# Kernel optimization log

Measured on AMD Instinct MI355X. Metric: run time of the kernel, lower is better.

Reference implementation:

```python
import jax, jax.numpy as jnp
import numpy as np

NUM_TOPICS = 50
NUM_TIMES = 12
VOCAB1 = 5000
VOCAB2 = 2000
T_HIDDEN = 400
RHO = 300
DELTA = 0.005
BATCH = 32


def setup_inputs() -> dict:
    key = jax.random.key(0)
    ks = jax.random.split(key, 16)
    s = 0.02
    V = VOCAB1 + VOCAB2
    d = {}
    d["bows"] = jax.random.uniform(ks[0], (BATCH, NUM_TIMES, V), jnp.float32)
    d["normalized_bows"] = jax.random.uniform(ks[1], (BATCH, NUM_TIMES, V), jnp.float32)
    d["qmap_w"] = jax.random.normal(ks[2], (T_HIDDEN, V), jnp.float32) * s
    d["qmap_b"] = jnp.zeros((T_HIDDEN,), jnp.float32)
    d["lstm_wih0"] = jax.random.normal(ks[3], (4 * T_HIDDEN, T_HIDDEN), jnp.float32) * s
    d["lstm_whh0"] = jax.random.normal(ks[4], (4 * T_HIDDEN, T_HIDDEN), jnp.float32) * s
    d["lstm_bih0"] = jnp.zeros((4 * T_HIDDEN,), jnp.float32)
    d["lstm_bhh0"] = jnp.zeros((4 * T_HIDDEN,), jnp.float32)
    d["lstm_wih1"] = jax.random.normal(ks[5], (4 * T_HIDDEN, T_HIDDEN), jnp.float32) * s
    d["lstm_whh1"] = jax.random.normal(ks[6], (4 * T_HIDDEN, T_HIDDEN), jnp.float32) * s
    d["lstm_bih1"] = jnp.zeros((4 * T_HIDDEN,), jnp.float32)
    d["lstm_bhh1"] = jnp.zeros((4 * T_HIDDEN,), jnp.float32)
    d["mu_theta_w"] = jax.random.normal(ks[7], (NUM_TOPICS, T_HIDDEN + NUM_TOPICS), jnp.float32) * s
    d["mu_theta_b"] = jnp.zeros((NUM_TOPICS,), jnp.float32)
    d["ls_theta_w"] = jax.random.normal(ks[8], (NUM_TOPICS, T_HIDDEN + NUM_TOPICS), jnp.float32) * s
    d["ls_theta_b"] = jnp.zeros((NUM_TOPICS,), jnp.float32)
    d["mu_q_alpha"] = jax.random.normal(ks[9], (NUM_TOPICS, NUM_TIMES, RHO), jnp.float32)
    d["logsigma_q_alpha"] = jax.random.normal(ks[10], (NUM_TOPICS, NUM_TIMES, RHO), jnp.float32)
    d["rho1_w"] = jax.random.normal(ks[11], (VOCAB1, RHO), jnp.float32) * s
    d["rho1_b"] = jnp.zeros((VOCAB1,), jnp.float32)
    d["rho2_w"] = jax.random.normal(ks[12], (VOCAB2, RHO), jnp.float32) * s
    d["rho2_b"] = jnp.zeros((VOCAB2,), jnp.float32)
    return d


def _kl(qm, qls, pm, pls):
    # 0.5 * sum_last[ (exp(qls) + (qm-pm)^2) / (exp(pls)+1e-6) - 1 + pls - qls ], mean over rest
    t = (jnp.exp(qls) + (qm - pm) ** 2) / (jnp.exp(pls) + 1e-6) - 1.0 + pls - qls
    return (0.5 * jnp.sum(t, axis=-1)).mean()


def _lstm(x, layers):
    # x: [B, T, H]; PyTorch gate order i, f, g, o; eval mode -> no inter-layer dropout
    for wih, whh, bih, bhh in layers:
        B = x.shape[0]
        H = whh.shape[1]

        def step(carry, xt, wih=wih, whh=whh, bih=bih, bhh=bhh):
            h, c = carry
            g = xt @ wih.T + bih + h @ whh.T + bhh
            i, f, gg, o = jnp.split(g, 4, axis=-1)
            c = jax.nn.sigmoid(f) * c + jax.nn.sigmoid(i) * jnp.tanh(gg)
            h = jax.nn.sigmoid(o) * jnp.tanh(c)
            return (h, c), h

        init = (jnp.zeros((B, H), x.dtype), jnp.zeros((B, H), x.dtype))
        _, hs = jax.lax.scan(step, init, jnp.swapaxes(x, 0, 1))  # [T, B, H]
        x = jnp.swapaxes(hs, 0, 1)
    return x


def _likelihood(beta, theta, bows_v, key):
    # beta: [T, K, V], theta: [T, B, K], bows_v: [B, T, V]
    def body(carry, xs):
        t, beta_t, theta_t, bows_t = xs
        # pi[b,v,k] = softmax_k( beta[k,v] * theta[b,k] )
        pi = jax.nn.softmax(theta_t[:, None, :] * beta_t.T[None, :, :], axis=-1)  # [B,V,K]
        g = jax.random.gumbel(jax.random.fold_in(key, t), pi.shape, pi.dtype)
        # F.gumbel_softmax with pi as the "logits", tau=1, hard=True (straight-through)
        y_soft = jax.nn.softmax(pi + g, axis=-1)
        y_hard = jax.nn.one_hot(jnp.argmax(y_soft, axis=-1), pi.shape[-1], dtype=pi.dtype)
        z = y_hard + y_soft - jax.lax.stop_gradient(y_soft)
        kld = (-(z * jnp.log(theta_t)[:, None, :]).sum(-1).mean()
               - (((pi * z).sum(-1) * (jnp.log(pi) * z).sum(-1)).sum(-1)).mean())
        beta_z = beta_t * z.mean(0).T   # [K, V]
        theta_z = theta_t * z.mean(1)   # [B, K]
        ll = (jnp.log(theta_z @ beta_z) * bows_t).sum(1).mean()
        return carry, (kld, ll)

    ts = jnp.arange(beta.shape[0])
    _, (klds, lls) = jax.lax.scan(jax.checkpoint(body), 0,
                                  (ts, beta, theta, jnp.swapaxes(bows_v, 0, 1)))
    return klds.sum(), lls.sum()


def _forward(bows, normalized_bows, qmap_w, qmap_b,
             lstm_wih0, lstm_whh0, lstm_bih0, lstm_bhh0,
             lstm_wih1, lstm_whh1, lstm_bih1, lstm_bhh1,
             mu_theta_w, mu_theta_b, ls_theta_w, ls_theta_b,
             mu_q_alpha, logsigma_q_alpha, rho1_w, rho1_b, rho2_w, rho2_b):
    B = bows.shape[0]
    log_delta = jnp.log(jnp.float32(DELTA))

    # ---- get_theta (eval mode: reparameterize -> mu, dropout off) ----
    inp = normalized_bows @ qmap_w.T + qmap_b                       # [B,T,H]
    out = _lstm(inp, [(lstm_wih0, lstm_whh0, lstm_bih0, lstm_bhh0),
                      (lstm_wih1, lstm_whh1, lstm_bih1, lstm_bhh1)])
    out_t = jnp.swapaxes(out, 0, 1)                                 # [T,B,H]
    inp0 = jnp.concatenate([out_t[0], jnp.zeros((B, NUM_TOPICS), out.dtype)], axis=-1)
    mu0 = inp0 @ mu_theta_w.T + mu_theta_b
    ls0 = inp0 @ ls_theta_w.T + ls_theta_b
    kl0 = _kl(mu0, ls0, jnp.zeros_like(mu0), jnp.zeros_like(ls0))

    def tstep(z_prev, o_t):
        inp_t = jnp.concatenate([o_t, z_prev], axis=-1)
        mu = inp_t @ mu_theta_w.T + mu_theta_b
        ls = inp_t @ ls_theta_w.T + ls_theta_b
        klt = _kl(mu, ls, z_prev, jnp.full_like(mu, log_delta))
        return mu, (mu, klt)

    _, (zs_rest, kls) = jax.lax.scan(tstep, mu0, out_t[1:])
    zs = jnp.concatenate([mu0[None], zs_rest], axis=0)              # [T,B,K]
    kld_theta = kl0 + kls.sum()
    theta = jax.nn.softmax(zs, axis=-1)

    # ---- get_alpha (eval mode: alpha_t = mu_q_alpha[:,t]) -> fully vectorized ----
    q_mu = jnp.swapaxes(mu_q_alpha, 0, 1)                           # [T,K,R]
    q_ls = jnp.swapaxes(logsigma_q_alpha, 0, 1)
    p_mu = jnp.concatenate([jnp.zeros_like(q_mu[:1]), q_mu[:-1]], axis=0)
    p_ls = jnp.concatenate([jnp.zeros_like(q_ls[:1]), jnp.full_like(q_ls[1:], log_delta)], axis=0)
    kl_tk = 0.5 * jnp.sum((jnp.exp(q_ls) + (q_mu - p_mu) ** 2) / (jnp.exp(p_ls) + 1e-6)
                          - 1.0 + p_ls - q_ls, axis=-1)             # [T,K]
    kld_alpha = kl_tk.mean(-1).sum()
    alpha = q_mu

    # ---- get_beta ----
    beta1 = jax.nn.softmax(jnp.einsum('tkr,vr->tkv', alpha, rho1_w) + rho1_b, axis=-1)
    beta2 = jax.nn.softmax(jnp.einsum('tkr,vr->tkv', alpha, rho2_w) + rho2_b, axis=-1)

    # ---- decode ----
    key = jax.random.key(42)
    kld_z1, ll1 = _likelihood(beta1, theta, bows[:, :, :VOCAB1], jax.random.fold_in(key, 1))
    kld_z2, ll2 = _likelihood(beta2, theta, bows[:, :, -VOCAB2:], jax.random.fold_in(key, 2))
    recon_loss = -ll1 - ll2
    return jnp.stack([recon_loss, kld_theta, kld_z1, kld_z2, kld_alpha])


def reference(bows, normalized_bows, qmap_w, qmap_b,
              lstm_wih0, lstm_whh0, lstm_bih0, lstm_bhh0,
              lstm_wih1, lstm_whh1, lstm_bih1, lstm_bhh1,
              mu_theta_w, mu_theta_b, ls_theta_w, ls_theta_b,
              mu_q_alpha, logsigma_q_alpha, rho1_w, rho1_b, rho2_w, rho2_b):
    return _forward(bows, normalized_bows, qmap_w, qmap_b,
                    lstm_wih0, lstm_whh0, lstm_bih0, lstm_bhh0,
                    lstm_wih1, lstm_whh1, lstm_bih1, lstm_bhh1,
                    mu_theta_w, mu_theta_b, ls_theta_w, ls_theta_b,
                    mu_q_alpha, logsigma_q_alpha, rho1_w, rho1_b, rho2_w, rho2_b)
```

## Files before the change

### kernel.cpp

```cpp
#include <hip/hip_runtime.h>

#define LOG_DELTA (-5.2983174f)
#define LOG50     (3.9120230054f)

typedef __attribute__((ext_vector_type(8))) short short8v;
typedef __attribute__((ext_vector_type(4))) float f32x4;

constexpr size_t OFF_C1G1  = 0;
constexpr size_t OFF_C1G2  = 19200;
constexpr size_t OFF_ACCS  = 38400;
constexpr size_t OFF_C0G   = 38416;
constexpr size_t OFF_BETA  = OFF_C0G  + 4200000;
constexpr size_t OFF_ALPHAT= OFF_BETA + 4200000;
constexpr size_t OFF_INP   = OFF_ALPHAT + 180000;
constexpr size_t OFF_X0    = OFF_INP  + 153600;
constexpr size_t OFF_OUT0  = OFF_X0   + 614400;
constexpr size_t OFF_X1    = OFF_OUT0 + 153600;
constexpr size_t OFF_OUT1  = OFF_X1   + 614400;
constexpr size_t OFF_CST   = OFF_OUT1 + 153600;
constexpr size_t OFF_MUH   = OFF_CST  + 12800;
constexpr size_t OFF_THETA = OFF_MUH  + 38400;
constexpr size_t OFF_LTH   = OFF_THETA+ 19200;
constexpr size_t OFF_MUW4  = OFF_LTH  + 19200;
constexpr size_t OFF_LSW4  = OFF_MUW4 + 20000;
constexpr size_t OFF_RS    = OFF_LTH  + 3300;
constexpr size_t OFF_W0P   = OFF_C0G;
constexpr size_t OFF_W1P   = OFF_C0G + 640000;
constexpr size_t OFF_WI1P  = OFF_C0G + 1280000;
constexpr size_t OFF_NBBF  = OFF_C0G + 1920000;
constexpr size_t OFF_R1BF  = OFF_C0G + 3271680;
constexpr size_t OFF_QWBF  = OFF_BETA;
constexpr size_t OFF_W0BF  = OFF_BETA + 1408000;
constexpr size_t OFF_CST1  = OFF_X1;
constexpr size_t OFF_ALBF  = OFF_X1 + 12800;
constexpr size_t OFF_R2BF  = OFF_X1 + 108800;

__device__ __forceinline__ float wsum64(float x){
  #pragma unroll
  for (int o = 32; o; o >>= 1) x += __shfl_down(x, o);
  return x;
}
__device__ __forceinline__ float u01(unsigned int x){
  x ^= x >> 16; x *= 0x7feb352dU;
  x ^= x >> 15; x *= 0x846ca68bU;
  x ^= x >> 16;
  return ((float)x + 0.5f) * (1.0f/4294967296.0f);
}
__device__ __forceinline__ unsigned short f2bf(float x){
  unsigned int u = __float_as_uint(x);
  u += 0x7FFFu + ((u >> 16) & 1u);
  return (unsigned short)(u >> 16);
}
__device__ __forceinline__ ushort4 f4bf(float4 v){
  ushort4 r;
  r.x = f2bf(v.x); r.y = f2bf(v.y); r.z = f2bf(v.z); r.w = f2bf(v.w);
  return r;
}

__global__ void prep_misc(float* __restrict__ ws,
    const float* __restrict__ muW, const float* __restrict__ lsW,
    const float* __restrict__ qmu,
    const float* __restrict__ bi0, const float* __restrict__ bh0,
    const float* __restrict__ bi1, const float* __restrict__ bh1,
    const float* __restrict__ mb,  const float* __restrict__ lb,
    const float* __restrict__ qb,
    const float* __restrict__ whh0, const float* __restrict__ whh1,
    const float* __restrict__ wih1,
    const float* __restrict__ nbows, const float* __restrict__ qmap_w,
    const float* __restrict__ wih0,
    const float* __restrict__ rho1w, const float* __restrict__ rho2w)
{
  float* zbase = ws + OFF_C1G1;
  float* muW4  = ws + OFF_MUW4;
  float* lsW4  = ws + OFF_LSW4;
  unsigned short* albf = (unsigned short*)(ws + OFF_ALBF);
  float* bsum0 = ws + OFF_LTH;
  float* bsum1 = ws + OFF_LTH + 1600;
  float* mlb   = ws + OFF_LTH + 3200;
  float* rs    = ws + OFF_RS;
  unsigned int* inbz = (unsigned int*)(ws + OFF_INP);
  float* inpf  = ws + OFF_ALPHAT;
  float* w0P   = ws + OFF_W0P;
  float* w1P   = ws + OFF_W1P;
  float* wi1P  = ws + OFF_WI1P;
  unsigned short* nbbf = (unsigned short*)(ws + OFF_NBBF);
  unsigned short* qwbf = (unsigned short*)(ws + OFF_QWBF);
  unsigned short* w0bf = (unsigned short*)(ws + OFF_W0BF);
  unsigned short* r1bf = (unsigned short*)(ws + OFF_R1BF);
  unsigned short* r2bf = (unsigned short*)(ws + OFF_R2BF);
  const float4 z4 = {0.f, 0.f, 0.f, 0.f};

  for (long long un = blockIdx.x*blockDim.x + threadIdx.x; un < 2713337LL;
       un += (long long)gridDim.x*blockDim.x){
    if (un < 9604){
      int j = (int)un * 4;
      if (j + 3 < 38416) *(float4*)&zbase[j] = z4;
      else { for (int q = 0; q < 4 && j+q < 38416; ++q) zbase[j+q] = 0.f; }
    }
    else if (un < 14604){
      int j = (int)(un - 9604) * 4;
      int k = j / 400, c = j % 400;
      const float* s = &muW[k*450 + c];
      float4 v = {s[0], s[1], s[2], s[3]};
      *(float4*)&muW4[j] = v;
    }
    else if (un < 19604){
      int j = (int)(un - 14604) * 4;
      int k = j / 400, c = j % 400;
      const float* s = &lsW[k*450 + c];
      float4 v = {s[0], s[1], s[2], s[3]};
      *(float4*)&lsW4[j] = v;
    }
    else if (un < 67604){
      int j = (int)(un - 19604) * 4;
      int m = j / 320, r = j % 320;
      int t = m / 50, k = m % 50;
      ushort4 o = {0,0,0,0};
      if (r < 300) o = f4bf(*(const float4*)&qmu[((size_t)k*12 + t)*300 + r]);
      *(ushort4*)&albf[j] = o;
    }
    else if (un < 68004){
      int j = (int)(un - 67604) * 4;
      float4 a = *(const float4*)&bi0[j], b = *(const float4*)&bh0[j];
      float4 v = {a.x+b.x, a.y+b.y, a.z+b.z, a.w+b.w};
      *(float4*)&bsum0[j] = v;
    }
    else if (un < 68404){
      int j = (int)(un - 68004) * 4;
      float4 a = *(const float4*)&bi1[j], b = *(const float4*)&bh1[j];
      float4 v = {a.x+b.x, a.y+b.y, a.z+b.z, a.w+b.w};
      *(float4*)&bsum1[j] = v;
    }
    else if (un < 68429){
      int j = (int)(un - 68404) * 4;
      #pragma unroll
      for (int q = 0; q < 4; ++q){
        int jj = j + q;
        mlb[jj] = (jj < 50) ? mb[jj] : lb[jj-50];
      }
    }
    else if (un < 68729){
      int j = (int)(un - 68429) * 4;
      *(float4*)&rs[j] = z4;
    }
    else if (un < 88697){
      int j = (int)(un - 68729) * 4;
      *(uint4*)&inbz[j] = make_uint4(0u,0u,0u,0u);
    }
    else if (un < 568697){
      long long rel = un - 88697;
      int half = (int)(rel / 160000);
      int j = (int)(rel % 160000) * 4;
      int ub = j / 3200, rem = j % 3200;
      int r = rem / 8, c = rem % 8;
      int ul = c >> 2;
      int u = ub*2 + ul;
      const float* src = (half == 0) ? whh0 : (half == 1) ? whh1 : wih1;
      float* dst = (half == 0) ? w0P : (half == 1) ? w1P : wi1P;
      float4 v = { src[((size_t)(0*400 + u))*400 + r],
                   src[((size_t)(1*400 + u))*400 + r],
                   src[((size_t)(2*400 + u))*400 + r],
                   src[((size_t)(3*400 + u))*400 + r] };
      *(float4*)&dst[j] = v;
    }
    else if (un < 1244537){
      int j = (int)(un - 568697) * 4;
      int row = j / 7040, v = j % 7040;
      ushort4 o = {0,0,0,0};
      if (v < 7000) o = f4bf(*(const float4*)&nbows[(size_t)row*7000 + v]);
      *(ushort4*)&nbbf[j] = o;
    }
    else if (un < 1948537){
      int j = (int)(un - 1244537) * 4;
      int row = j / 7040, v = j % 7040;
      ushort4 o = {0,0,0,0};
      if (v < 7000) o = f4bf(*(const float4*)&qmap_w[(size_t)row*7000 + v]);
      *(ushort4*)&qwbf[j] = o;
    }
    else if (un < 2114937){
      int j = (int)(un - 1948537) * 4;
      int row = j / 416, r = j % 416;
      ushort4 o = {0,0,0,0};
      if (r < 400) o = f4bf(*(const float4*)&wih0[(size_t)row*400 + r]);
      *(ushort4*)&w0bf[j] = o;
    }
    else if (un < 2514937){
      int j = (int)(un - 2114937) * 4;
      int row = j / 320, r = j % 320;
      ushort4 o = {0,0,0,0};
      if (r < 300) o = f4bf(*(const float4*)&rho1w[(size_t)row*300 + r]);
      *(ushort4*)&r1bf[j] = o;
    }
    else if (un < 2674937){
      int j = (int)(un - 2514937) * 4;
      int row = j / 320, r = j % 320;
      ushort4 o = {0,0,0,0};
      if (r < 300) o = f4bf(*(const float4*)&rho2w[(size_t)row*300 + r]);
      *(ushort4*)&r2bf[j] = o;
    }
    else {
      int j = (int)(un - 2674937) * 4;
      int c = j % 400;
      *(float4*)&inpf[j] = *(const float4*)&qb[c];
    }
  }
}

__global__ __launch_bounds__(256) void gemm_bf16(
    const unsigned short* __restrict__ A, int lda,
    const unsigned short* __restrict__ B, int ldb,
    float* __restrict__ Cf, unsigned short* __restrict__ Cbf,
    float* __restrict__ Cacc, int ldc,
    int M, int N, int Kp, int kchunk,
    const float* __restrict__ bias, float* __restrict__ rowsum)
{
  __shared__ unsigned short As[64][40];
  __shared__ unsigned short Bs[64][40];
  __shared__ float sexp[64];
  const int tid = threadIdx.x;
  const int m0 = blockIdx.y * 64, n0 = blockIdx.x * 64;
  const int kbeg = blockIdx.z * kchunk;
  const int kend = min(Kp, kbeg + kchunk);
  const int wave = tid >> 6, lane = tid & 63;
  const int wm = (wave >> 1) * 32, wn = (wave & 1) * 32;
  const int ra = tid >> 2, ck = (tid & 3) << 3;
  const int fr = lane & 15, fo = (lane >> 4) << 3;
  if (rowsum && tid < 64) sexp[tid] = 0.f;

  f32x4 acc00 = {0.f,0.f,0.f,0.f}, acc01 = {0.f,0.f,0.f,0.f};
  f32x4 acc10 = {0.f,0.f,0.f,0.f}, acc11 = {0.f,0.f,0.f,0.f};
  int4 pa, pb;
  {
    int rA = m0 + ra, rB = n0 + ra;
    pa = (rA < M) ? *(const int4*)&A[(size_t)rA*lda + kbeg + ck] : make_int4(0,0,0,0);
    pb = (rB < N) ? *(const int4*)&B[(size_t)rB*ldb + kbeg + ck] : make_int4(0,0,0,0);
  }
  for (int k0 = kbeg; k0 < kend; k0 += 32){
    *(int4*)&As[ra][ck] = pa;
    *(int4*)&Bs[ra][ck] = pb;
    __syncthreads();
    if (k0 + 32 < kend){
      int rA = m0 + ra, rB = n0 + ra;
      pa = (rA < M) ? *(const int4*)&A[(size_t)rA*lda + k0 + 32 + ck] : make_int4(0,0,0,0);
      pb = (rB < N) ? *(const int4*)&B[(size_t)rB*ldb + k0 + 32 + ck] : make_int4(0,0,0,0);
    }
    short8v a0 = *(const short8v*)&As[wm      + fr][fo];
    short8v a1 = *(const short8v*)&As[wm + 16 + fr][fo];
    short8v b0 = *(const short8v*)&Bs[wn      + fr][fo];
    short8v b1 = *(const short8v*)&Bs[wn + 16 + fr][fo];
    acc00 = __builtin_amdgcn_mfma_f32_16x16x32_bf16(a0, b0, acc00, 0, 0, 0);
    acc01 = __builtin_amdgcn_mfma_f32_16x16x32_bf16(a0, b1, acc01, 0, 0, 0);
    acc10 = __builtin_amdgcn_mfma_f32_16x16x32_bf16(a1, b0, acc10, 0, 0, 0);
    acc11 = __builtin_amdgcn_mfma_f32_16x16x32_bf16(a1, b1, acc11, 0, 0, 0);
    __syncthreads();
  }
  const int rbase = (lane >> 4) << 2;
  auto epi = [&](f32x4 ac0, f32x4 ac1, int mi){
    #pragma unroll
    for (int reg = 0; reg < 4; ++reg){
      const int lr = wm + mi*16 + rbase + reg;
      const int gr = m0 + lr;
      float ex = 0.f;
      {
        int gc = n0 + wn + fr;
        if (gr < M && gc < N){
          if (Cacc) atomicAdd(&Cacc[(size_t)gr*ldc + gc], ac0[reg]);
          else {
            float val = ac0[reg] + (bias ? bias[gc] : 0.f);
            if (Cbf) Cbf[(size_t)gr*ldc + gc] = f2bf(val);
            else     Cf [(size_t)gr*ldc + gc] = val;
            if (rowsum) ex += __expf(val);
          }
        }
      }
      {
        int gc = n0 + wn + 16 + fr;
        if (gr < M && gc < N){
          if (Cacc) atomicAdd(&Cacc[(size_t)gr*ldc + gc], ac1[reg]);
          else {
            float val = ac1[reg] + (bias ? bias[gc] : 0.f);
            if (Cbf) Cbf[(size_t)gr*ldc + gc] = f2bf(val);
            else     Cf [(size_t)gr*ldc + gc] = val;
            if (rowsum) ex += __expf(val);
          }
        }
      }
      if (rowsum){
        ex += __shfl_xor(ex, 1); ex += __shfl_xor(ex, 2);
        ex += __shfl_xor(ex, 4); ex += __shfl_xor(ex, 8);
        if (fr == 0 && gr < M) atomicAdd(&sexp[lr], ex);
      }
    }
  };
  epi(acc00, acc01, 0);
  epi(acc10, acc11, 1);
  if (rowsum){
    __syncthreads();
    if (tid < 64 && m0 + tid < M) atomicAdd(&rowsum[m0 + tid], sexp[tid]);
  }
}

__global__ void cvt_inp(const float* __restrict__ inpf, unsigned short* __restrict__ inpbf){
  int un = blockIdx.x*blockDim.x + threadIdx.x;
  if (un < 38400){
    int j = un * 4;
    int r = j / 400, c = j % 400;
    ushort4 o = f4bf(*(const float4*)&inpf[j]);
    *(ushort4*)&inpbf[r*416 + c] = o;
  }
}

__device__ __forceinline__ float4 g4(const float* __restrict__ base, int row, int nrows,
                                     int ld, int k, int kend){
  float4 v; v.x = v.y = v.z = v.w = 0.f;
  if (row < nrows){
    const float* q = base + (size_t)row*ld + k;
    if (k + 3 < kend) v = *(const float4*)q;
  }
  return v;
}
__global__ __launch_bounds__(256) void gemm_f32(
    const float* __restrict__ A, int lda,
    const float* __restrict__ B, int ldb,
    float* __restrict__ C, int ldc,
    int M, int N, int K,
    const float* __restrict__ bias)
{
  __shared__ __align__(16) float As[16][68];
  __shared__ __align__(16) float Bs[16][68];
  const int tid = threadIdx.x;
  const int m0 = blockIdx.y * 64, n0 = blockIdx.x * 64;
  const int lm  = tid >> 2;
  const int lkq = (tid & 3) << 2;
  const int ty = tid >> 4, tx = tid & 15;
  float acc[4][4];
  #pragma unroll
  for (int i=0;i<4;++i)
    #pragma unroll
    for (int j=0;j<4;++j) acc[i][j] = 0.f;
  for (int k0 = 0; k0 < K; k0 += 16){
    float4 av = g4(A, m0+lm, M, lda, k0+lkq, K);
    float4 bv = g4(B, n0+lm, N, ldb, k0+lkq, K);
    As[lkq+0][lm]=av.x; As[lkq+1][lm]=av.y; As[lkq+2][lm]=av.z; As[lkq+3][lm]=av.w;
    Bs[lkq+0][lm]=bv.x; Bs[lkq+1][lm]=bv.y; Bs[lkq+2][lm]=bv.z; Bs[lkq+3][lm]=bv.w;
    __syncthreads();
    #pragma unroll
    for (int kk = 0; kk < 16; ++kk){
      const float4 a = *(const float4*)&As[kk][ty<<2];
      const float4 b = *(const float4*)&Bs[kk][tx<<2];
      float ar[4] = {a.x,a.y,a.z,a.w};
      float br[4] = {b.x,b.y,b.z,b.w};
      #pragma unroll
      for (int i=0;i<4;++i)
        #pragma unroll
        for (int j=0;j<4;++j) acc[i][j] = fmaf(ar[i], br[j], acc[i][j]);
    }
    __syncthreads();
  }
  const int om = m0 + (ty<<2), on = n0 + (tx<<2);
  #pragma unroll
  for (int i=0;i<4;++i)
    #pragma unroll
    for (int j=0;j<4;++j)
      if (om+i < M && on+j < N)
        C[(size_t)(om+i)*ldc + (on+j)] = acc[i][j] + (bias ? bias[on+j] : 0.f);
}

__global__ __launch_bounds__(256) void lstm_pipe(
    const float* __restrict__ X0,    const float* __restrict__ w0P,
    const float* __restrict__ wi1P,  const float* __restrict__ w1P,
    const float* __restrict__ bsum1,
    float* __restrict__ hs0, float* __restrict__ hs1,
    float* __restrict__ cst0, float* __restrict__ cst1, int step)
{
  __shared__ __align__(16) float4 hq4[100*32];
  __shared__ __align__(16) float4 wq4[400*2];
  __shared__ __align__(16) float4 red4[4][32][2];
  const int tid = threadIdx.x;
  const int rh = tid >> 6;
  const int b  = (tid & 63) >> 1;
  const int ul = tid & 1;
  const int rq0 = rh * 25;

  if (blockIdx.x < 200){
    const int t = step;
    if (t >= 12) return;
    const int ub = blockIdx.x;
    const int U0 = ub * 2;
    if (t > 0){
      for (int i = tid; i < 3200; i += 256){
        int bb = i & 31, rq = i >> 5;
        hq4[rq*32 + bb] = *(const float4*)&hs0[((size_t)(bb*12 + (t-1)))*400 + rq*4];
      }
      for (int i = tid; i < 800; i += 256)
        wq4[i] = *(const float4*)&w0P[(size_t)ub*3200 + i*4];
      __syncthreads();
      float4 acc = {0.f,0.f,0.f,0.f};
      #pragma unroll 5
      for (int rq = rq0; rq < rq0 + 25; ++rq){
        float4 h4 = hq4[rq*32 + b];
        float hr[4] = {h4.x, h4.y, h4.z, h4.w};
        #pragma unroll
        for (int dr = 0; dr < 4; ++dr){
          float4 w4 = wq4[(rq*4 + dr)*2 + ul];
          acc.x = fmaf(hr[dr], w4.x, acc.x);
          acc.y = fmaf(hr[dr], w4.y, acc.y);
          acc.z = fmaf(hr[dr], w4.z, acc.z);
          acc.w = fmaf(hr[dr], w4.w, acc.w);
        }
      }
      red4[rh][b][ul] = acc;
    }
    __syncthreads();
    if (tid < 64){
      const int bb = tid >> 1, uu = U0 + (tid & 1);
      float4 a = {0.f,0.f,0.f,0.f};
      if (t > 0){
        #pragma unroll
        for (int w = 0; w < 4; ++w){
          float4 r = red4[w][bb][tid & 1];
          a.x += r.x; a.y += r.y; a.z += r.z; a.w += r.w;
        }
      }
      const size_t xrow = ((size_t)bb*12 + t)*1600;
      float gi = a.x + X0[xrow          + uu];
      float gf = a.y + X0[xrow +  400   + uu];
      float gg = a.z + X0[xrow +  800   + uu];
      float go = a.w + X0[xrow + 1200   + uu];
      float ii = 1.f/(1.f + expf(-gi));
      float ff = 1.f/(1.f + expf(-gf));
      float tg = tanhf(gg);
      float oo = 1.f/(1.f + expf(-go));
      float c = (t == 0) ? 0.f : cst0[bb*400 + uu];
      c = ff*c + ii*tg;
      cst0[bb*400 + uu] = c;
      hs0[((size_t)bb*12 + t)*400 + uu] = oo * tanhf(c);
    }
  } else {
    const int t = step - 1;
    if (t < 0) return;
    const int ub = blockIdx.x - 200;
    const int U0 = ub * 2;
    float4 acc = {0.f,0.f,0.f,0.f};
    for (int i = tid; i < 3200; i += 256){
      int bb = i & 31, rq = i >> 5;
      hq4[rq*32 + bb] = *(const float4*)&hs0[((size_t)(bb*12 + t))*400 + rq*4];
    }
    for (int i = tid; i < 800; i += 256)
      wq4[i] = *(const float4*)&wi1P[(size_t)ub*3200 + i*4];
    __syncthreads();
    {
      #pragma unroll 5
      for (int rq = rq0; rq < rq0 + 25; ++rq){
        float4 h4 = hq4[rq*32 + b];
        float hr[4] = {h4.x, h4.y, h4.z, h4.w};
        #pragma unroll
        for (int dr = 0; dr < 4; ++dr){
          float4 w4 = wq4[(rq*4 + dr)*2 + ul];
          acc.x = fmaf(hr[dr], w4.x, acc.x);
          acc.y = fmaf(hr[dr], w4.y, acc.y);
          acc.z = fmaf(hr[dr], w4.z, acc.z);
          acc.w = fmaf(hr[dr], w4.w, acc.w);
        }
      }
    }
    __syncthreads();
    if (t > 0){
      for (int i = tid; i < 3200; i += 256){
        int bb = i & 31, rq = i >> 5;
        hq4[rq*32 + bb] = *(const float4*)&hs1[((size_t)(bb*12 + (t-1)))*400 + rq*4];
      }
      for (int i = tid; i < 800; i += 256)
        wq4[i] = *(const float4*)&w1P[(size_t)ub*3200 + i*4];
    }
    __syncthreads();
    if (t > 0){
      #pragma unroll 5
      for (int rq = rq0; rq < rq0 + 25; ++rq){
        float4 h4 = hq4[rq*32 + b];
        float hr[4] = {h4.x, h4.y, h4.z, h4.w};
        #pragma unroll
        for (int dr = 0; dr < 4; ++dr){
          float4 w4 = wq4[(rq*4 + dr)*2 + ul];
          acc.x = fmaf(hr[dr], w4.x, acc.x);
          acc.y = fmaf(hr[dr], w4.y, acc.y);
          acc.z = fmaf(hr[dr], w4.z, acc.z);
          acc.w = fmaf(hr[dr], w4.w, acc.w);
        }
      }
    }
    red4[rh][b][ul] = acc;
    __syncthreads();
    if (tid < 64){
      const int bb = tid >> 1, uu = U0 + (tid & 1);
      float4 a = {0.f,0.f,0.f,0.f};
      #pragma unroll
      for (int w = 0; w < 4; ++w){
        float4 r = red4[w][bb][tid & 1];
        a.x += r.x; a.y += r.y; a.z += r.z; a.w += r.w;
      }
      float gi = a.x + bsum1[        uu];
      float gf = a.y + bsum1[ 400 + uu];
      float gg = a.z + bsum1[ 800 + uu];
      float go = a.w + bsum1[1200 + uu];
      float ii = 1.f/(1.f + expf(-gi));
      float ff = 1.f/(1.f + expf(-gf));
      float tg = tanhf(gg);
      float oo = 1.f/(1.f + expf(-go));
      float c = (t == 0) ? 0.f : cst1[bb*400 + uu];
      c = ff*c + ii*tg;
      cst1[bb*400 + uu] = c;
      hs1[((size_t)bb*12 + t)*400 + uu] = oo * tanhf(c);
    }
  }
}

__global__ __launch_bounds__(64) void theta_par(
    const float* __restrict__ muH2,
    const float* __restrict__ muW, const float* __restrict__ lsW,
    float* __restrict__ theta, float* __restrict__ accs)
{
  __shared__ float wm[50][51], wl[50][51];
  __shared__ float zs[12][50];
  const int tid = threadIdx.x;
  const int b = blockIdx.x;
  for (int i = tid; i < 2500; i += 64){
    int k = i / 50, j = i % 50;
    wm[k][j] = muW[k*450 + 400 + j];
    wl[k][j] = lsW[k*450 + 400 + j];
  }
  __syncthreads();
  const float dd = expf(LOG_DELTA) + 1e-6f;
  float kacc = 0.f;
  for (int t = 0; t < 12; ++t){
    float kpart = 0.f;
    if (tid < 50){
      int k = tid;
      float m = muH2[((size_t)b*12 + t)*100 + k];
      float l = muH2[((size_t)b*12 + t)*100 + 50 + k];
      float zp = 0.f;
      if (t > 0){
        zp = zs[t-1][k];
        float sm = 0.f, sl = 0.f;
        #pragma unroll 5
        for (int j = 0; j < 50; ++j){
          float z = zs[t-1][j];
          sm = fmaf(z, wm[k][j], sm);
          sl = fmaf(z, wl[k][j], sl);
        }
        m += sm; l += sl;
      }
      zs[t][k] = m;
      float denom = (t > 0) ? dd : (1.f + 1e-6f);
      float pls = (t > 0) ? LOG_DELTA : 0.f;
      float d = m - zp;
      kpart = (expf(l) + d*d)/denom - 1.f + pls - l;
    }
    kpart = wsum64(kpart);
    if (tid == 0) kacc += 0.5f * kpart / 32.f;
    __syncthreads();
  }
  if (tid < 12){
    int t = tid;
    float m = -3.0e38f;
    for (int k = 0; k < 50; ++k) m = fmaxf(m, zs[t][k]);
    float S = 0.f;
    for (int k = 0; k < 50; ++k) S += expf(zs[t][k] - m);
    float inv = 1.f/S;
    for (int k = 0; k < 50; ++k)
      theta[((size_t)t*32 + b)*50 + k] = expf(zs[t][k] - m) * inv;
  }
  if (tid == 0) atomicAdd(&accs[6], kacc);
}

__global__ void kld_alpha_k(const float* __restrict__ qmu, const float* __restrict__ qls,
                            float* __restrict__ accs){
  const int t = blockIdx.x / 50, k = blockIdx.x % 50;
  const size_t base  = ((size_t)k*12 + t)*300;
  const size_t pbase = ((size_t)k*12 + (t-1))*300;
  const float dd  = (t > 0) ? (expf(LOG_DELTA) + 1e-6f) : (1.f + 1e-6f);
  const float pls = (t > 0) ? LOG_DELTA : 0.f;
  float s = 0.f;
  for (int r = threadIdx.x; r < 300; r += 64){
    float qm = qmu[base + r], ql = qls[base + r];
    float pm = (t > 0) ? qmu[pbase + r] : 0.f;
    float d = qm - pm;
    s += (expf(ql) + d*d)/dd - 1.f + pls - ql;
  }
  s = wsum64(s);
  if (threadIdx.x == 0) atomicAdd(&accs[7], 0.5f * s / 50.f);
}

__global__ __launch_bounds__(256) void pass1(
    const float* __restrict__ blog, const float* __restrict__ rs,
    const float* __restrict__ theta,
    float* __restrict__ bzg,
    unsigned int* __restrict__ c1u,
    float* __restrict__ accs)
{
  const int t = blockIdx.y;
  const int v0 = blockIdx.x * 64;
  __shared__ float th[32][50];
  __shared__ __align__(16) float be[50][64];
  __shared__ unsigned int c0p[64][13];
  __shared__ unsigned int c1p[2][32][25];
  __shared__ float rlog[2][50];
  __shared__ float kred[4];
  const int tid = threadIdx.x;

  if (tid < 100){
    int p = tid / 50, k = tid % 50;
    rlog[p][k] = __logf(rs[p*600 + t*50 + k]);
  }
  float lg[13];
  #pragma unroll
  for (int j = 0; j < 13; ++j){
    int i = tid + j*256;
    lg[j] = -40.f;
    if (i < 3200){
      int k = i >> 6, vl = i & 63, v = v0 + vl;
      if (v < 7000) lg[j] = blog[((size_t)t*50 + k)*7000 + v];
    }
  }
  #pragma unroll
  for (int j = 0; j < 7; ++j){
    int i = tid + j*256;
    if (i < 1600) th[i/50][i%50] = theta[(size_t)t*1600 + i];
  }
  for (int i = tid; i < 832; i += 256) ((unsigned int*)c0p)[i] = 0u;
  #pragma unroll
  for (int j = 0; j < 7; ++j){
    int i = tid + j*256;
    if (i < 1600) ((unsigned int*)c1p)[i] = 0u;
  }
  if (tid < 4) kred[tid] = 0.f;
  __syncthreads();
  #pragma unroll
  for (int j = 0; j < 13; ++j){
    int i = tid + j*256;
    if (i < 3200){
      int k = i >> 6, vl = i & 63, v = v0 + vl;
      int p = (v >= 5000);
      be[k][vl] = __expf(lg[j] - rlog[p][k]);
    }
  }
  __syncthreads();

  const int b = tid >> 3, sub = tid & 7;
  int off[8];
  #pragma unroll
  for (int i = 0; i < 8; ++i) off[i] = ((i >> 2) ? 32 : 0) + sub*4 + (i & 3);

  float sx[8], mx[8];
  #pragma unroll
  for (int i = 0; i < 8; ++i){ sx[i] = 0.f; mx[i] = 0.f; }
  for (int k = 0; k < 50; ++k){
    float tk = th[b][k];
    float4 q0 = *(const float4*)&be[k][sub*4];
    float4 q1 = *(const float4*)&be[k][32 + sub*4];
    float bv[8] = {q0.x,q0.y,q0.z,q0.w,q1.x,q1.y,q1.z,q1.w};
    #pragma unroll
    for (int i = 0; i < 8; ++i){
      float x = tk * bv[i];
      sx[i] += x;
      mx[i] = fmaxf(mx[i], x);
    }
  }
  float inv[8], lS1[8], bnd[8];
  #pragma unroll
  for (int i = 0; i < 8; ++i){
    inv[i] = 1.f / (50.f + sx[i]);
    lS1[i] = LOG50 + sx[i] * 0.02f;
    bnd[i] = (1.f + mx[i]) * inv[i];
  }

  int ks[8]; float xs[8];
  unsigned fmask = 0;
  const int sbase = (t*32 + b)*7000 + v0;
  #pragma unroll
  for (int i = 0; i < 8; ++i){
    ks[i] = 0; xs[i] = 0.f;
    if (v0 + off[i] >= 7000) fmask |= 1u << i;
  }
  int round = 0;
  while (true){
    const unsigned roff = (unsigned)round * 0x9E3779B9u;
    #pragma unroll
    for (int i = 0; i < 8; ++i){
      if (!((fmask >> i) & 1u)){
        const unsigned bse = (unsigned)(sbase + off[i]) * 2u;
        float u1 = u01(bse + roff);
        float u2 = u01(bse + 1u + roff);
        int kp = min((int)(u1 * 50.f), 49);
        float x  = th[b][kp] * be[kp][off[i]];
        float pi = (1.f + x) * inv[i];
        float y  = pi - bnd[i];
        float ap = 1.f + y + 0.5f*y*y;
        if (u2 <= ap || round >= 7){
          ks[i] = kp; xs[i] = x; fmask |= 1u << i;
        }
      }
    }
    ++round;
    if (__all(fmask == 255u)) break;
  }

  float kA1 = 0.f, kB1 = 0.f, kA2 = 0.f, kB2 = 0.f;
  #pragma unroll
  for (int i = 0; i < 8; ++i){
    const int vl = off[i], v = v0 + vl;
    if (v < 7000){
      float pis  = (1.f + xs[i]) * inv[i];
      float lpis = xs[i] - lS1[i];
      float lt   = __logf(th[b][ks[i]]);
      if (v >= 5000){ kA2 += lt; kB2 += pis*lpis; }
      else          { kA1 += lt; kB1 += pis*lpis; }
      atomicAdd(&c0p[vl][ks[i] >> 2], 1u << (8*(ks[i] & 3)));
      atomicAdd(&c1p[(v >= 5000) ? 1 : 0][b][ks[i] >> 1],
                (ks[i] & 1) ? 65536u : 1u);
    }
  }
  kA1 = wsum64(kA1); kB1 = wsum64(kB1); kA2 = wsum64(kA2); kB2 = wsum64(kB2);
  if ((tid & 63) == 0){
    atomicAdd(&kred[0], kA1); atomicAdd(&kred[1], kB1);
    atomicAdd(&kred[2], kA2); atomicAdd(&kred[3], kB2);
  }
  __syncthreads();
  #pragma unroll
  for (int j = 0; j < 13; ++j){
    int i = tid + j*256;
    if (i < 3200){
      int k = i >> 6, vl = i & 63, v = v0 + vl;
      if (v < 7000){
        float cnt = (float)((c0p[vl][k >> 2] >> (8*(k & 3))) & 0xFFu);
        bzg[(size_t)t*350000 + (size_t)k*7000 + v] = be[k][vl] * cnt * (1.f/32.f);
      }
    }
  }
  for (int i = tid; i < 1600; i += 256){
    int b2 = i / 50, k2 = i % 50;
    unsigned w1 = c1p[0][b2][k2 >> 1];
    unsigned w2 = c1p[1][b2][k2 >> 1];
    unsigned cnt1 = (k2 & 1) ? (w1 >> 16) : (w1 & 0xFFFFu);
    unsigned cnt2 = (k2 & 1) ? (w2 >> 16) : (w2 & 0xFFFFu);
    unsigned comb = cnt1 | (cnt2 << 16);
    if (comb) atomicAdd(&c1u[(size_t)t*1600 + i], comb);
  }
  if (tid < 4) atomicAdd(&accs[tid], kred[tid]);
}

__global__ __launch_bounds__(256) void pass2(
    const float* __restrict__ bzg, const float* __restrict__ theta,
    const unsigned int* __restrict__ c1u,
    const float* __restrict__ bows, float* __restrict__ accs)
{
  const int t = blockIdx.y, v0 = blockIdx.x * 64;
  __shared__ float tz[2][32][50];
  __shared__ __align__(16) float bzs[50][64];
  __shared__ float sr[2];
  const int tid = threadIdx.x;
  if (tid < 2) sr[tid] = 0.f;
  for (int i = tid; i < 1600; i += 256){
    int b = i / 50, k = i % 50;
    float th_ = theta[(size_t)t*1600 + i];
    unsigned cw = c1u[(size_t)t*1600 + i];
    tz[0][b][k] = th_ * (float)(cw & 0xFFFFu) * (1.f/5000.f);
    tz[1][b][k] = th_ * (float)(cw >> 16)     * (1.f/2000.f);
  }
  for (int i = tid; i < 3200; i += 256){
    int k = i >> 6, vl = i & 63, v = v0 + vl;
    bzs[k][vl] = (v < 7000) ? bzg[(size_t)t*350000 + (size_t)k*7000 + v] : 0.f;
  }
  __syncthreads();

  const int b = tid >> 3, sub = tid & 7;
  int off[8];
  #pragma unroll
  for (int i = 0; i < 8; ++i) off[i] = ((i >> 2) ? 32 : 0) + sub*4 + (i & 3);
  int part[8];
  #pragma unroll
  for (int i = 0; i < 8; ++i) part[i] = (v0 + off[i] >= 5000);
  float dot[8];
  #pragma unroll
  for (int i = 0; i < 8; ++i) dot[i] = 0.f;
  for (int k = 0; k < 50; ++k){
    float t0 = tz[0][b][k], t1 = tz[1][b][k];
    float4 q0 = *(const float4*)&bzs[k][sub*4];
    float4 q1 = *(const float4*)&bzs[k][32 + sub*4];
    float bv[8] = {q0.x,q0.y,q0.z,q0.w,q1.x,q1.y,q1.z,q1.w};
    #pragma unroll
    for (int i = 0; i < 8; ++i)
      dot[i] = fmaf(part[i] ? t1 : t0, bv[i], dot[i]);
  }
  float w8[8];
  const size_t brow = ((size_t)b*12 + t)*7000;
  if (v0 + 63 < 7000){
    float4 wa = *(const float4*)&bows[brow + v0 + sub*4];
    float4 wb = *(const float4*)&bows[brow + v0 + 32 + sub*4];
    w8[0]=wa.x; w8[1]=wa.y; w8[2]=wa.z; w8[3]=wa.w;
    w8[4]=wb.x; w8[5]=wb.y; w8[6]=wb.z; w8[7]=wb.w;
  } else {
    #pragma unroll
    for (int i = 0; i < 8; ++i)
      w8[i] = (v0 + off[i] < 7000) ? bows[brow + v0 + off[i]] : 0.f;
  }
  float s1 = 0.f, s2 = 0.f;
  #pragma unroll
  for (int i = 0; i < 8; ++i){
    const int v = v0 + off[i];
    if (v < 7000){
      const float l = __logf(dot[i]) * w8[i];
      if (part[i]) s2 += l; else s1 += l;
    }
  }
  s1 = wsum64(s1); s2 = wsum64(s2);
  if ((tid & 63) == 0){ atomicAdd(&sr[0], s1); atomicAdd(&sr[1], s2); }
  __syncthreads();
  if (tid < 2) atomicAdd(&accs[4 + tid], sr[tid]);
}

__global__ void finalize_k(const float* __restrict__ accs, float* __restrict__ out){
  if (threadIdx.x == 0 && blockIdx.x == 0){
    out[0] = -(accs[4] + accs[5]) * (1.f/32.f);
    out[1] = accs[6];
    out[2] = -accs[0]/(32.f*5000.f) - accs[1]/32.f;
    out[3] = -accs[2]/(32.f*2000.f) - accs[3]/32.f;
    out[4] = accs[7];
  }
}

extern "C" void kernel_launch(void* const* d_in, const int* in_sizes, int n_in,
                              void* d_out, int out_size, void* d_ws, size_t ws_size,
                              hipStream_t stream)
{
  const float* bows   = (const float*)d_in[0];
  const float* nbows  = (const float*)d_in[1];
  const float* qmap_w = (const float*)d_in[2];
  const float* qmap_b = (const float*)d_in[3];
  const float* wih0   = (const float*)d_in[4];
  const float* whh0   = (const float*)d_in[5];
  const float* bih0   = (const float*)d_in[6];
  const float* bhh0   = (const float*)d_in[7];
  const float* wih1   = (const float*)d_in[8];
  const float* whh1   = (const float*)d_in[9];
  const float* bih1   = (const float*)d_in[10];
  const float* bhh1   = (const float*)d_in[11];
  const float* muW    = (const float*)d_in[12];
  const float* muB    = (const float*)d_in[13];
  const float* lsW    = (const float*)d_in[14];
  const float* lsB    = (const float*)d_in[15];
  const float* qmu    = (const float*)d_in[16];
  const float* qlsa   = (const float*)d_in[17];
  const float* rho1w  = (const float*)d_in[18];
  const float* rho1b  = (const float*)d_in[19];
  const float* rho2w  = (const float*)d_in[20];
  const float* rho2b  = (const float*)d_in[21];

  float* ws  = (float*)d_ws;
  float* out = (float*)d_out;

  unsigned int* c1u = (unsigned int*)(ws + OFF_C1G1);
  float* accs  = ws + OFF_ACCS;
  float* bzg   = ws + OFF_C0G;
  float* beta  = ws + OFF_BETA;
  float* inpf  = ws + OFF_ALPHAT;
  float* X0    = ws + OFF_X0;
  float* hs0   = ws + OFF_OUT0;
  float* hs1   = ws + OFF_OUT1;
  float* cst0  = ws + OFF_CST;
  float* cst1  = ws + OFF_CST1;
  float* muH2  = ws + OFF_MUH;
  float* theta = ws + OFF_THETA;
  float* muW4  = ws + OFF_MUW4;
  float* bsum0 = ws + OFF_LTH;
  float* bsum1 = ws + OFF_LTH + 1600;
  float* mlb   = ws + OFF_LTH + 3200;
  float* rs    = ws + OFF_RS;
  unsigned short* nbbf  = (unsigned short*)(ws + OFF_NBBF);
  unsigned short* qwbf  = (unsigned short*)(ws + OFF_QWBF);
  unsigned short* inpbf = (unsigned short*)(ws + OFF_INP);
  unsigned short* w0bf  = (unsigned short*)(ws + OFF_W0BF);
  unsigned short* albf  = (unsigned short*)(ws + OFF_ALBF);
  unsigned short* r1bf  = (unsigned short*)(ws + OFF_R1BF);
  unsigned short* r2bf  = (unsigned short*)(ws + OFF_R2BF);
  float* w0P  = ws + OFF_W0P;
  float* w1P  = ws + OFF_W1P;
  float* wi1P = ws + OFF_WI1P;

  prep_misc<<<2048, 256, 0, stream>>>(ws, muW, lsW, qmu, bih0, bhh0, bih1, bhh1,
                                      muB, lsB, qmap_b, whh0, whh1, wih1,
                                      nbows, qmap_w, wih0, rho1w, rho2w);
  kld_alpha_k<<<600, 64, 0, stream>>>(qmu, qlsa, accs);

  gemm_bf16<<<dim3(7,6,10), 256, 0, stream>>>(nbbf, 7040, qwbf, 7040,
                                              nullptr, nullptr, inpf, 400,
                                              384, 400, 7040, 704, nullptr, nullptr);
  cvt_inp<<<150, 256, 0, stream>>>(inpf, inpbf);

  gemm_bf16<<<dim3(25,6,1), 256, 0, stream>>>(inpbf, 416, w0bf, 416,
                                              X0, nullptr, nullptr, 1600,
                                              384, 1600, 416, 416, bsum0, nullptr);
  for (int i = 0; i < 13; ++i)
    lstm_pipe<<<400, 256, 0, stream>>>(X0, w0P, wi1P, w1P, bsum1,
                                       hs0, hs1, cst0, cst1, i);

  gemm_f32<<<dim3(2,6), 256, 0, stream>>>(hs1, 400, muW4, 400, muH2, 100,
                                          384, 100, 400, mlb);
  theta_par<<<32, 64, 0, stream>>>(muH2, muW, lsW, theta, accs);

  gemm_bf16<<<dim3(79,10,1), 256, 0, stream>>>(albf, 320, r1bf, 320,
                                               beta, nullptr, nullptr, 7000,
                                               600, 5000, 320, 320, rho1b, rs);
  gemm_bf16<<<dim3(32,10,1), 256, 0, stream>>>(albf, 320, r2bf, 320,
                                               beta + 5000, nullptr, nullptr, 7000,
                                               600, 2000, 320, 320, rho2b, rs + 600);

  pass1<<<dim3(110,12), 256, 0, stream>>>(beta, rs, theta, bzg, c1u, accs);
  pass2<<<dim3(110,12), 256, 0, stream>>>(bzg, theta, c1u, bows, accs);

  finalize_k<<<1, 64, 0, stream>>>(accs, out);
}
```

Before: 391.6 us.

## Fuse KL-alpha into prep kernel, store LSTM hidden and bzg as bf16

Three separate changes. The kld_alpha kernel is folded into extra blocks of prep_misc, which write per-block partials that finalize_k reduces, and the zeroing range is narrowed to match. The LSTM hidden-state tile in shared memory becomes bf16, cutting its LDS footprint and read traffic. The pass1-to-pass2 intermediate bzg is written as bf16 to halve that global round trip. These remove one launch and some memory traffic at the cost of lower precision in the recurrence and likelihood terms.

```diff
diff --git a/kernel.cpp b/kernel.cpp
--- a/kernel.cpp
+++ b/kernel.cpp
@@ -7,7 +7,7 @@
 typedef __attribute__((ext_vector_type(4))) float f32x4;
 
 constexpr size_t OFF_C1G1  = 0;
-constexpr size_t OFF_C1G2  = 19200;
+constexpr size_t OFF_KLDP  = 19200;
 constexpr size_t OFF_ACCS  = 38400;
 constexpr size_t OFF_C0G   = 38416;
 constexpr size_t OFF_BETA  = OFF_C0G  + 4200000;
@@ -51,6 +51,9 @@
   u += 0x7FFFu + ((u >> 16) & 1u);
   return (unsigned short)(u >> 16);
 }
+__device__ __forceinline__ float bf2f(unsigned short u){
+  return __uint_as_float(((unsigned int)u) << 16);
+}
 __device__ __forceinline__ ushort4 f4bf(float4 v){
   ushort4 r;
   r.x = f2bf(v.x); r.y = f2bf(v.y); r.z = f2bf(v.z); r.w = f2bf(v.w);
@@ -59,7 +62,7 @@
 
 __global__ void prep_misc(float* __restrict__ ws,
     const float* __restrict__ muW, const float* __restrict__ lsW,
-    const float* __restrict__ qmu,
+    const float* __restrict__ qmu, const float* __restrict__ qls,
     const float* __restrict__ bi0, const float* __restrict__ bh0,
     const float* __restrict__ bi1, const float* __restrict__ bh1,
     const float* __restrict__ mb,  const float* __restrict__ lb,
@@ -70,6 +73,29 @@
     const float* __restrict__ wih0,
     const float* __restrict__ rho1w, const float* __restrict__ rho2w)
 {
+  const int tid = threadIdx.x;
+  if (blockIdx.x >= 2048){
+    float* kldp = ws + OFF_KLDP;
+    const int bid2 = blockIdx.x - 2048;
+    const int t = bid2 / 50, k = bid2 % 50;
+    if (tid < 64){
+      const size_t base  = ((size_t)k*12 + t)*300;
+      const size_t pbase = ((size_t)k*12 + (t-1))*300;
+      const float dd  = (t > 0) ? (expf(LOG_DELTA) + 1e-6f) : (1.f + 1e-6f);
+      const float pls = (t > 0) ? LOG_DELTA : 0.f;
+      float s = 0.f;
+      for (int r = tid; r < 300; r += 64){
+        float qm = qmu[base + r], ql = qls[base + r];
+        float pm = (t > 0) ? qmu[pbase + r] : 0.f;
+        float d = qm - pm;
+        s += (expf(ql) + d*d)/dd - 1.f + pls - ql;
+      }
+      s = wsum64(s);
+      if (tid == 0) kldp[bid2] = 0.5f * s / 50.f;
+    }
+    return;
+  }
+
   float* zbase = ws + OFF_C1G1;
   float* muW4  = ws + OFF_MUW4;
   float* lsW4  = ws + OFF_LSW4;
@@ -89,66 +115,68 @@
   unsigned short* r1bf = (unsigned short*)(ws + OFF_R1BF);
   unsigned short* r2bf = (unsigned short*)(ws + OFF_R2BF);
   const float4 z4 = {0.f, 0.f, 0.f, 0.f};
-
-  for (long long un = blockIdx.x*blockDim.x + threadIdx.x; un < 2713337LL;
-       un += (long long)gridDim.x*blockDim.x){
-    if (un < 9604){
+  for (long long un = (long long)blockIdx.x*256 + tid; un < 2708537LL;
+       un += 2048LL*256){
+    if (un < 4800){
       int j = (int)un * 4;
-      if (j + 3 < 38416) *(float4*)&zbase[j] = z4;
-      else { for (int q = 0; q < 4 && j+q < 38416; ++q) zbase[j+q] = 0.f; }
-    }
-    else if (un < 14604){
-      int j = (int)(un - 9604) * 4;
+      *(float4*)&zbase[j] = z4;
+    }
+    else if (un < 4804){
+      int j = (int)(un - 4800) * 4;
+      *(float4*)&ws[OFF_ACCS + j] = z4;
+    }
+    else if (un < 9804){
+      int j = (int)(un - 4804) * 4;
       int k = j / 400, c = j % 400;
       const float* s = &muW[k*450 + c];
       float4 v = {s[0], s[1], s[2], s[3]};
       *(float4*)&muW4[j] = v;
     }
-    else if (un < 19604){
-      int j = (int)(un - 14604) * 4;
+    else if (un < 14804){
+      int j = (int)(un - 9804) * 4;
       int k = j / 400, c = j % 400;
       const float* s = &lsW[k*450 + c];
       float4 v = {s[0], s[1], s[2], s[3]};
       *(float4*)&lsW4[j] = v;
     }
-    else if (un < 67604){
-      int j = (int)(un - 19604) * 4;
+    else if (un < 62804){
+      int j = (int)(un - 14804) * 4;
       int m = j / 320, r = j % 320;
       int t = m / 50, k = m % 50;
       ushort4 o = {0,0,0,0};
       if (r < 300) o = f4bf(*(const float4*)&qmu[((size_t)k*12 + t)*300 + r]);
       *(ushort4*)&albf[j] = o;
     }
-    else if (un < 68004){
-      int j = (int)(un - 67604) * 4;
+    else if (un < 63204){
+      int j = (int)(un - 62804) * 4;
       float4 a = *(const float4*)&bi0[j], b = *(const float4*)&bh0[j];
       float4 v = {a.x+b.x, a.y+b.y, a.z+b.z, a.w+b.w};
       *(float4*)&bsum0[j] = v;
     }
-    else if (un < 68404){
-      int j = (int)(un - 68004) * 4;
+    else if (un < 63604){
+      int j = (int)(un - 63204) * 4;
       float4 a = *(const float4*)&bi1[j], b = *(const float4*)&bh1[j];
       float4 v = {a.x+b.x, a.y+b.y, a.z+b.z, a.w+b.w};
       *(float4*)&bsum1[j] = v;
     }
-    else if (un < 68429){
-      int j = (int)(un - 68404) * 4;
+    else if (un < 63629){
+      int j = (int)(un - 63604) * 4;
       #pragma unroll
       for (int q = 0; q < 4; ++q){
         int jj = j + q;
         mlb[jj] = (jj < 50) ? mb[jj] : lb[jj-50];
       }
     }
-    else if (un < 68729){
-      int j = (int)(un - 68429) * 4;
+    else if (un < 63929){
+      int j = (int)(un - 63629) * 4;
       *(float4*)&rs[j] = z4;
     }
-    else if (un < 88697){
-      int j = (int)(un - 68729) * 4;
+    else if (un < 83897){
+      int j = (int)(un - 63929) * 4;
       *(uint4*)&inbz[j] = make_uint4(0u,0u,0u,0u);
     }
-    else if (un < 568697){
-      long long rel = un - 88697;
+    else if (un < 563897){
+      long long rel = un - 83897;
       int half = (int)(rel / 160000);
       int j = (int)(rel % 160000) * 4;
       int ub = j / 3200, rem = j % 3200;
@@ -163,43 +191,43 @@
                    src[((size_t)(3*400 + u))*400 + r] };
       *(float4*)&dst[j] = v;
     }
-    else if (un < 1244537){
-      int j = (int)(un - 568697) * 4;
+    else if (un < 1239737){
+      int j = (int)(un - 563897) * 4;
       int row = j / 7040, v = j % 7040;
       ushort4 o = {0,0,0,0};
       if (v < 7000) o = f4bf(*(const float4*)&nbows[(size_t)row*7000 + v]);
       *(ushort4*)&nbbf[j] = o;
     }
-    else if (un < 1948537){
-      int j = (int)(un - 1244537) * 4;
+    else if (un < 1943737){
+      int j = (int)(un - 1239737) * 4;
       int row = j / 7040, v = j % 7040;
       ushort4 o = {0,0,0,0};
       if (v < 7000) o = f4bf(*(const float4*)&qmap_w[(size_t)row*7000 + v]);
       *(ushort4*)&qwbf[j] = o;
     }
-    else if (un < 2114937){
-      int j = (int)(un - 1948537) * 4;
+    else if (un < 2110137){
+      int j = (int)(un - 1943737) * 4;
       int row = j / 416, r = j % 416;
       ushort4 o = {0,0,0,0};
       if (r < 400) o = f4bf(*(const float4*)&wih0[(size_t)row*400 + r]);
       *(ushort4*)&w0bf[j] = o;
     }
-    else if (un < 2514937){
-      int j = (int)(un - 2114937) * 4;
+    else if (un < 2510137){
+      int j = (int)(un - 2110137) * 4;
       int row = j / 320, r = j % 320;
       ushort4 o = {0,0,0,0};
       if (r < 300) o = f4bf(*(const float4*)&rho1w[(size_t)row*300 + r]);
       *(ushort4*)&r1bf[j] = o;
     }
-    else if (un < 2674937){
-      int j = (int)(un - 2514937) * 4;
+    else if (un < 2670137){
+      int j = (int)(un - 2510137) * 4;
       int row = j / 320, r = j % 320;
       ushort4 o = {0,0,0,0};
       if (r < 300) o = f4bf(*(const float4*)&rho2w[(size_t)row*300 + r]);
       *(ushort4*)&r2bf[j] = o;
     }
     else {
-      int j = (int)(un - 2674937) * 4;
+      int j = (int)(un - 2670137) * 4;
       int c = j % 400;
       *(float4*)&inpf[j] = *(const float4*)&qb[c];
     }
@@ -373,7 +401,7 @@
     float* __restrict__ hs0, float* __restrict__ hs1,
     float* __restrict__ cst0, float* __restrict__ cst1, int step)
 {
-  __shared__ __align__(16) float4 hq4[100*32];
+  __shared__ __align__(16) ushort4 hqb[100*32];
   __shared__ __align__(16) float4 wq4[400*2];
   __shared__ __align__(16) float4 red4[4][32][2];
   const int tid = threadIdx.x;
@@ -390,7 +418,7 @@
     if (t > 0){
       for (int i = tid; i < 3200; i += 256){
         int bb = i & 31, rq = i >> 5;
-        hq4[rq*32 + bb] = *(const float4*)&hs0[((size_t)(bb*12 + (t-1)))*400 + rq*4];
+        hqb[rq*32 + bb] = f4bf(*(const float4*)&hs0[((size_t)(bb*12 + (t-1)))*400 + rq*4]);
       }
       for (int i = tid; i < 800; i += 256)
         wq4[i] = *(const float4*)&w0P[(size_t)ub*3200 + i*4];
@@ -398,8 +426,8 @@
       float4 acc = {0.f,0.f,0.f,0.f};
       #pragma unroll 5
       for (int rq = rq0; rq < rq0 + 25; ++rq){
-        float4 h4 = hq4[rq*32 + b];
-        float hr[4] = {h4.x, h4.y, h4.z, h4.w};
+        ushort4 h4 = hqb[rq*32 + b];
+        float hr[4] = {bf2f(h4.x), bf2f(h4.y), bf2f(h4.z), bf2f(h4.w)};
         #pragma unroll
         for (int dr = 0; dr < 4; ++dr){
           float4 w4 = wq4[(rq*4 + dr)*2 + ul];
@@ -444,7 +472,7 @@
     float4 acc = {0.f,0.f,0.f,0.f};
     for (int i = tid; i < 3200; i += 256){
       int bb = i & 31, rq = i >> 5;
-      hq4[rq*32 + bb] = *(const float4*)&hs0[((size_t)(bb*12 + t))*400 + rq*4];
+      hqb[rq*32 + bb] = f4bf(*(const float4*)&hs0[((size_t)(bb*12 + t))*400 + rq*4]);
     }
     for (int i = tid; i < 800; i += 256)
       wq4[i] = *(const float4*)&wi1P[(size_t)ub*3200 + i*4];
@@ -452,8 +480,8 @@
     {
       #pragma unroll 5
       for (int rq = rq0; rq < rq0 + 25; ++rq){
-        float4 h4 = hq4[rq*32 + b];
-        float hr[4] = {h4.x, h4.y, h4.z, h4.w};
+        ushort4 h4 = hqb[rq*32 + b];
+        float hr[4] = {bf2f(h4.x), bf2f(h4.y), bf2f(h4.z), bf2f(h4.w)};
         #pragma unroll
         for (int dr = 0; dr < 4; ++dr){
           float4 w4 = wq4[(rq*4 + dr)*2 + ul];
@@ -468,7 +496,7 @@
     if (t > 0){
       for (int i = tid; i < 3200; i += 256){
         int bb = i & 31, rq = i >> 5;
-        hq4[rq*32 + bb] = *(const float4*)&hs1[((size_t)(bb*12 + (t-1)))*400 + rq*4];
+        hqb[rq*32 + bb] = f4bf(*(const float4*)&hs1[((size_t)(bb*12 + (t-1)))*400 + rq*4]);
       }
       for (int i = tid; i < 800; i += 256)
         wq4[i] = *(const float4*)&w1P[(size_t)ub*3200 + i*4];
@@ -477,8 +505,8 @@
     if (t > 0){
       #pragma unroll 5
       for (int rq = rq0; rq < rq0 + 25; ++rq){
-        float4 h4 = hq4[rq*32 + b];
-        float hr[4] = {h4.x, h4.y, h4.z, h4.w};
+        ushort4 h4 = hqb[rq*32 + b];
+        float hr[4] = {bf2f(h4.x), bf2f(h4.y), bf2f(h4.z), bf2f(h4.w)};
         #pragma unroll
         for (int dr = 0; dr < 4; ++dr){
           float4 w4 = wq4[(rq*4 + dr)*2 + ul];
@@ -573,28 +601,10 @@
   if (tid == 0) atomicAdd(&accs[6], kacc);
 }
 
-__global__ void kld_alpha_k(const float* __restrict__ qmu, const float* __restrict__ qls,
-                            float* __restrict__ accs){
-  const int t = blockIdx.x / 50, k = blockIdx.x % 50;
-  const size_t base  = ((size_t)k*12 + t)*300;
-  const size_t pbase = ((size_t)k*12 + (t-1))*300;
-  const float dd  = (t > 0) ? (expf(LOG_DELTA) + 1e-6f) : (1.f + 1e-6f);
-  const float pls = (t > 0) ? LOG_DELTA : 0.f;
-  float s = 0.f;
-  for (int r = threadIdx.x; r < 300; r += 64){
-    float qm = qmu[base + r], ql = qls[base + r];
-    float pm = (t > 0) ? qmu[pbase + r] : 0.f;
-    float d = qm - pm;
-    s += (expf(ql) + d*d)/dd - 1.f + pls - ql;
-  }
-  s = wsum64(s);
-  if (threadIdx.x == 0) atomicAdd(&accs[7], 0.5f * s / 50.f);
-}
-
 __global__ __launch_bounds__(256) void pass1(
     const float* __restrict__ blog, const float* __restrict__ rs,
     const float* __restrict__ theta,
-    float* __restrict__ bzg,
+    unsigned short* __restrict__ bzg,
     unsigned int* __restrict__ c1u,
     float* __restrict__ accs)
 {
@@ -733,7 +743,7 @@
       int k = i >> 6, vl = i & 63, v = v0 + vl;
       if (v < 7000){
         float cnt = (float)((c0p[vl][k >> 2] >> (8*(k & 3))) & 0xFFu);
-        bzg[(size_t)t*350000 + (size_t)k*7000 + v] = be[k][vl] * cnt * (1.f/32.f);
+        bzg[(size_t)t*350000 + (size_t)k*7000 + v] = f2bf(be[k][vl] * cnt * (1.f/32.f));
       }
     }
   }
@@ -750,7 +760,7 @@
 }
 
 __global__ __launch_bounds__(256) void pass2(
-    const float* __restrict__ bzg, const float* __restrict__ theta,
+    const unsigned short* __restrict__ bzg, const float* __restrict__ theta,
     const unsigned int* __restrict__ c1u,
     const float* __restrict__ bows, float* __restrict__ accs)
 {
@@ -769,7 +779,7 @@
   }
   for (int i = tid; i < 3200; i += 256){
     int k = i >> 6, vl = i & 63, v = v0 + vl;
-    bzs[k][vl] = (v < 7000) ? bzg[(size_t)t*350000 + (size_t)k*7000 + v] : 0.f;
+    bzs[k][vl] = (v < 7000) ? bf2f(bzg[(size_t)t*350000 + (size_t)k*7000 + v]) : 0.f;
   }
   __syncthreads();
 
@@ -819,13 +829,19 @@
   if (tid < 2) atomicAdd(&accs[4 + tid], sr[tid]);
 }
 
-__global__ void finalize_k(const float* __restrict__ accs, float* __restrict__ out){
-  if (threadIdx.x == 0 && blockIdx.x == 0){
+__global__ void finalize_k(const float* __restrict__ accs,
+                           const float* __restrict__ kldp,
+                           float* __restrict__ out){
+  const int tid = threadIdx.x;
+  float s = 0.f;
+  for (int i = tid; i < 600; i += 64) s += kldp[i];
+  s = wsum64(s);
+  if (tid == 0){
     out[0] = -(accs[4] + accs[5]) * (1.f/32.f);
     out[1] = accs[6];
     out[2] = -accs[0]/(32.f*5000.f) - accs[1]/32.f;
     out[3] = -accs[2]/(32.f*2000.f) - accs[3]/32.f;
-    out[4] = accs[7];
+    out[4] = s;
   }
 }
 
@@ -860,8 +876,9 @@
   float* out = (float*)d_out;
 
   unsigned int* c1u = (unsigned int*)(ws + OFF_C1G1);
+  float* kldp  = ws + OFF_KLDP;
   float* accs  = ws + OFF_ACCS;
-  float* bzg   = ws + OFF_C0G;
+  unsigned short* bzg = (unsigned short*)(ws + OFF_C0G);
   float* beta  = ws + OFF_BETA;
   float* inpf  = ws + OFF_ALPHAT;
   float* X0    = ws + OFF_X0;
@@ -887,10 +904,10 @@
   float* w1P  = ws + OFF_W1P;
   float* wi1P = ws + OFF_WI1P;
 
-  prep_misc<<<2048, 256, 0, stream>>>(ws, muW, lsW, qmu, bih0, bhh0, bih1, bhh1,
-                                      muB, lsB, qmap_b, whh0, whh1, wih1,
+  prep_misc<<<2648, 256, 0, stream>>>(ws, muW, lsW, qmu, qlsa, bih0, bhh0,
+                                      bih1, bhh1, muB, lsB, qmap_b,
+                                      whh0, whh1, wih1,
                                       nbows, qmap_w, wih0, rho1w, rho2w);
-  kld_alpha_k<<<600, 64, 0, stream>>>(qmu, qlsa, accs);
 
   gemm_bf16<<<dim3(7,6,10), 256, 0, stream>>>(nbbf, 7040, qwbf, 7040,
                                               nullptr, nullptr, inpf, 400,
@@ -918,5 +935,5 @@
   pass1<<<dim3(110,12), 256, 0, stream>>>(beta, rs, theta, bzg, c1u, accs);
   pass2<<<dim3(110,12), 256, 0, stream>>>(bzg, theta, c1u, bows, accs);
 
-  finalize_k<<<1, 64, 0, stream>>>(accs, out);
-}
+  finalize_k<<<1, 64, 0, stream>>>(accs, kldp, out);
+}
```

After: 392.2 us. No clear change (+0.2%).
